# Kernel optimization log

Measured on AMD Instinct MI355X. Metric: run time of the kernel, lower is better.

The kernel has to match this reference:

```python
import jax, jax.numpy as jnp
import numpy as np
import itertools

DIM = 9  # LUT resolution per axis
B, C, H, W = 4, 5, 1024, 1024


def setup_inputs() -> dict:
    key = jax.random.key(0)
    k1, k2 = jax.random.split(key)
    x = jax.random.uniform(k1, (B, C, H, W), dtype=jnp.float32)  # pixel values in [0,1]
    LUT = jax.random.normal(k2, (1, 5, DIM, DIM, DIM, DIM, DIM), dtype=jnp.float32)
    return {"x": x, "LUT": LUT}


def _pglut_transform(x, LUT):
    # x: [B,5,H,W] in [0,1]; LUT: [1,5,dim,dim,dim,dim,dim]
    dim = LUT.shape[2]
    scale = jnp.float32(dim - 1)
    xs = x * scale                                   # [B,5,H,W]
    idx = jnp.clip(jnp.floor(xs), 0, dim - 2).astype(jnp.int32)
    frac = xs - idx.astype(x.dtype)                  # [B,5,H,W], in [0,1]

    lut_flat = LUT[0].reshape(5, dim ** 5)           # [5, dim^5]
    # flattened base index of the lower corner of the hypercube: [B,H,W]
    base = sum(idx[:, d] * int(dim ** (4 - d)) for d in range(5))

    out = jnp.zeros((5,) + base.shape, x.dtype)      # [5,B,H,W]
    for corner in itertools.product((0, 1), repeat=5):
        offset = sum(c * int(dim ** (4 - d)) for d, c in enumerate(corner))
        # quinlinear weight: prod_d (frac_d if corner else 1-frac_d)
        w = jnp.ones(base.shape, x.dtype)
        for d, c in enumerate(corner):
            w = w * (frac[:, d] if c else (1.0 - frac[:, d]))
        vals = lut_flat[:, base + offset]            # gather -> [5,B,H,W]
        out = out + w[None] * vals
    return jnp.transpose(out, (1, 0, 2, 3))          # [B,5,H,W]


def reference(x, LUT):
    return _pglut_transform(x, LUT)
```

## Files before the change

### kernel.cpp

```cpp
#include <hip/hip_runtime.h>
#include <hip/hip_fp16.h>


#define HW_    (1024 * 1024)
#define NPIX   (4 * HW_)
#define LUTC   59049
#define NBIN   512
#define CAP    8704
#define OVFCAP 65536
#define PXB    4096
#define NCELL2 (9 * 9 * 8 * 8 * 8)
#define OVF_IDX 1023

#define R_BYTES   ((size_t)NCELL2 * 80)
#define PAY_ENT   ((size_t)NBIN * CAP + OVFCAP)
#define PAY_BYTES (PAY_ENT * 16)
#define POS_BYTES ((size_t)NPIX * 4)
#define OFF_R    ((size_t)0)
#define OFF_PAY  (OFF_R + R_BYTES)
#define OFF_POS  (OFF_PAY + PAY_BYTES)
#define OFF_CNT  (OFF_POS + POS_BYTES)
#define CNT_BYTES ((size_t)4096)
#define WS_NEED  (OFF_CNT + CNT_BYTES)

typedef _Float16 v2h __attribute__((ext_vector_type(2)));
typedef float    f4v __attribute__((ext_vector_type(4)));
union H2U { __half2 h; uint u; v2h v; };
union H8U { uint4 q; __half2 h2[4]; };
union HQ8 { __half h[8]; uint4 q; };

__global__ __launch_bounds__(256) void k1_buildR(
    const float* __restrict__ lut, __half* __restrict__ R)
{
    __shared__ float s[5 * 162];
    int bid = blockIdx.x;
    int i2 = bid & 7;
    int r  = bid >> 3;
    int Q  = r * 9 + i2;
    const int fb = Q * 81;
    for (int u = threadIdx.x; u < 5 * 162; u += 256) {
        int c = u / 162; int j = u - c * 162;
        s[u] = lut[(size_t)c * LUTC + fb + j];
    }
    __syncthreads();
    int cellBaseG = bid * 64;
    for (int t = threadIdx.x; t < 320; t += 256) {
        int cell = t / 5; int c = t - cell * 5;
        int i3 = cell >> 3, i4 = cell & 7;
        const float* L = s + c * 162 + i3 * 9 + i4;
        HQ8 u;
        u.h[0] = __float2half(L[0]);   u.h[1] = __float2half(L[81]);
        u.h[2] = __float2half(L[1]);   u.h[3] = __float2half(L[82]);
        u.h[4] = __float2half(L[9]);   u.h[5] = __float2half(L[90]);
        u.h[6] = __float2half(L[10]);  u.h[7] = __float2half(L[91]);
        ((uint4*)R)[(size_t)(cellBaseG + cell) * 5 + c] = u.q;
    }
}

__global__ __launch_bounds__(1024) void k4_fused(
    const float* __restrict__ x,
    uint* __restrict__ gcnt,
    uint4* __restrict__ pay, uint* __restrict__ sortpos)
{
    __shared__ uint4  sPay[PXB];
    __shared__ uint   sStart[NBIN];
    __shared__ uint   sCur[NBIN];
    __shared__ uint   sCB[NBIN];
    __shared__ uint   sWsum[8];

    int tid = threadIdx.x, blk = blockIdx.x;
    if (tid < NBIN) sCur[tid] = 0;
    __syncthreads();

    int pBase = blk * PXB + tid * 4;
    int b = pBase >> 20, hw = pBase & (HW_ - 1);
    const float* xp = x + (size_t)b * 5 * HW_ + hw;
    f4v xv[5];
    #pragma unroll
    for (int d = 0; d < 5; ++d)
        xv[d] = __builtin_nontemporal_load((const f4v*)(xp + (size_t)d * HW_));

    uint4 plr[4]; uint keyr[4];
    #pragma unroll
    for (int j = 0; j < 4; ++j) {
        float f[5]; int idx[5];
        #pragma unroll
        for (int d = 0; d < 5; ++d) {
            float xs = xv[d][j] * 8.0f;
            int i = (int)floorf(xs); i = i < 0 ? 0 : (i > 7 ? 7 : i);
            idx[d] = i; f[d] = xs - (float)i;
        }
        int key   = (idx[0] << 6) | (idx[1] << 3) | idx[2];
        int local = (idx[3] << 3) | idx[4];
        H2U a, bq, c;
        a.h  = __float22half2_rn(make_float2(f[0], f[1]));
        bq.h = __float22half2_rn(make_float2(f[2], f[3]));
        c.h  = __float22half2_rn(make_float2(f[4], 0.f));
        plr[j].x = a.u; plr[j].y = bq.u; plr[j].z = c.u;
        plr[j].w = (uint)(pBase + j) | ((uint)local << 22);
        keyr[j] = (uint)key;
        atomicAdd(&sCur[key], 1u);
    }
    __syncthreads();

    uint v = 0, s = 0, base = 0;
    if (tid < NBIN) {
        v = sCur[tid];
        if (v) base = atomicAdd(&gcnt[tid * 2], v);
        s = v;
        #pragma unroll
        for (int off = 1; off < 64; off <<= 1) {
            uint t = __shfl_up(s, off);
            if ((tid & 63) >= off) s += t;
        }
        if ((tid & 63) == 63) sWsum[tid >> 6] = s;
    }
    __syncthreads();
    if (tid < NBIN) {
        uint add = 0;
        #pragma unroll
        for (int w = 0; w < 8; ++w)
            add += (w < (tid >> 6)) ? sWsum[w] : 0u;
        sStart[tid] = s + add - v;
        sCB[tid]    = base;
        sCur[tid]   = 0;
    }
    __syncthreads();

    uint dstr[4];
    #pragma unroll
    for (int j = 0; j < 4; ++j) {
        uint key  = keyr[j];
        uint rank = atomicAdd(&sCur[key], 1u);
        uint slot = sStart[key] + rank;
        sPay[slot] = plr[j];
        uint gIdx = sCB[key] + rank;
        uint dst;
        if (gIdx < CAP) {
            dst = key * CAP + gIdx;
        } else {
            uint oi = atomicAdd(&gcnt[OVF_IDX], 1u);
            if (oi >= OVFCAP) oi = OVFCAP - 1;
            pay[(size_t)NBIN * CAP + oi] = plr[j];
            dst = (uint)(NBIN * CAP) + oi;
        }
        dstr[j] = dst;
    }
    *(uint4*)(sortpos + pBase) = make_uint4(dstr[0], dstr[1], dstr[2], dstr[3]);
    __syncthreads();

    if (tid < NBIN) {
        uint cnt = sCur[tid];
        uint st  = sStart[tid];
        uint cb  = sCB[tid];
        uint4* gp = pay + (size_t)tid * CAP;
        #pragma unroll 2
        for (uint j = 0; j < cnt; ++j) {
            uint gIdx = cb + j;
            if (gIdx < CAP)
                gp[gIdx] = sPay[st + j];
        }
    }
}

__global__ __launch_bounds__(256, 7) void k5_compute(
    const __half* __restrict__ R, const uint* __restrict__ gcnt,
    uint4* __restrict__ pay)
{
    __shared__ uint4 stbl[1280];
    int bid = blockIdx.x;
    int bin = bid >> 2, q = bid & 3;
    int i0 = bin >> 6, i1 = (bin >> 3) & 7, i2 = bin & 7;
    const uint4* R4 = (const uint4*)R;
    #pragma unroll
    for (int slab = 0; slab < 4; ++slab) {
        int a = slab >> 1, bcorner = slab & 1;
        size_t srcBase = (size_t)((((i0 + a) * 9 + (i1 + bcorner)) * 8 + i2) * 64) * 5;
        for (int rr = threadIdx.x; rr < 320; rr += 256)
            stbl[slab * 320 + rr] = R4[srcBase + rr];
    }
    __syncthreads();
    uint n = gcnt[bin * 2]; if (n > CAP) n = CAP;
    uint B0 = (uint)bin * CAP;
    uint st = B0 + ((n * q) >> 2), en = B0 + ((n * (q + 1)) >> 2);
    for (uint i = st + threadIdx.x; i < en; i += 256) {
        uint4 pl = pay[i];
        H2U f01, f23, f4x; f01.u = pl.x; f23.u = pl.y; f4x.u = pl.z;
        float2 F01 = __half22float2(f01.h);
        float2 F23 = __half22float2(f23.h);
        float f0 = F01.x, f1 = F01.y, f2 = F23.x;
        __half2 f33 = __half2half2(__high2half(f23.h));
        __half2 f44 = __half2half2(__low2half(f4x.h));
        int local = (int)(pl.w >> 22);
        const uint4* cbase = stbl + local * 5;
        float g0 = 1.f - f0, g1 = 1.f - f1, g2 = 1.f - f2;
        H2U wv[4];
        float w00 = g0 * g1, w01c = g0 * f1, w10 = f0 * g1, w11 = f0 * f1;
        wv[0].h = __float22half2_rn(make_float2(w00  * g2, w00  * f2));
        wv[1].h = __float22half2_rn(make_float2(w01c * g2, w01c * f2));
        wv[2].h = __float22half2_rn(make_float2(w10  * g2, w10  * f2));
        wv[3].h = __float22half2_rn(make_float2(w11  * g2, w11  * f2));
        float acc[5];
        #pragma unroll
        for (int c = 0; c < 5; ++c) acc[c] = 0.f;
        #pragma unroll
        for (int slab = 0; slab < 4; ++slab) {
            #pragma unroll
            for (int c = 0; c < 5; ++c) {
                H8U u; u.q = cbase[slab * 320 + c];
                __half2 e0 = __hfma2(f44, __hsub2(u.h2[1], u.h2[0]), u.h2[0]);
                __half2 e1 = __hfma2(f44, __hsub2(u.h2[3], u.h2[2]), u.h2[2]);
                H2U dd; dd.h = __hfma2(f33, __hsub2(e1, e0), e0);
#if __has_builtin(__builtin_amdgcn_fdot2)
                acc[c] = __builtin_amdgcn_fdot2(dd.v, wv[slab].v, acc[c], false);
#else
                float2 D = __half22float2(dd.h);
                float2 W = __half22float2(wv[slab].h);
                acc[c] = fmaf(D.x, W.x, fmaf(D.y, W.y, acc[c]));
#endif
            }
        }
        H2U o01, o23, o4x;
        o01.h = __float22half2_rn(make_float2(acc[0], acc[1]));
        o23.h = __float22half2_rn(make_float2(acc[2], acc[3]));
        o4x.h = __float22half2_rn(make_float2(acc[4], 0.f));
        uint4 res; res.x = o01.u; res.y = o23.u; res.z = o4x.u; res.w = pl.w;
        pay[i] = res;
    }
}

__global__ __launch_bounds__(256) void k5_ovf(
    const float* __restrict__ x, const __half* __restrict__ R,
    const uint* __restrict__ gcnt, uint4* __restrict__ pay)
{
    uint n = gcnt[OVF_IDX]; if (n > OVFCAP) n = OVFCAP;
    for (uint i = blockIdx.x * 256 + threadIdx.x; i < n; i += 64 * 256) {
        uint4 pl = pay[(size_t)NBIN * CAP + i];
        uint p = pl.w & 0x3FFFFFu;
        int b = p >> 20, hw = p & (HW_ - 1);
        const float* xp = x + (size_t)b * 5 * HW_ + hw;
        float f[5]; int idx[5];
        #pragma unroll
        for (int d = 0; d < 5; ++d) {
            float xs = xp[(size_t)d * HW_] * 8.0f;
            int ii = (int)floorf(xs); ii = ii < 0 ? 0 : (ii > 7 ? 7 : ii);
            idx[d] = ii; f[d] = xs - (float)ii;
        }
        float g0 = 1.f - f[0], g1 = 1.f - f[1];
        float f2 = f[2], f3 = f[3], f4 = f[4];
        int cellBase = ((idx[0] * 9 + idx[1]) * 8 + idx[2]) * 64 + idx[3] * 8 + idx[4];
        float acc[5];
        #pragma unroll
        for (int c = 0; c < 5; ++c) acc[c] = 0.f;
        #pragma unroll
        for (int c0 = 0; c0 < 2; ++c0) {
            float w0 = c0 ? f[0] : g0;
            int o0 = cellBase + c0 * 4608;
            #pragma unroll
            for (int c1 = 0; c1 < 2; ++c1) {
                float w = w0 * (c1 ? f[1] : g1);
                const uint4* pc = (const uint4*)R + (size_t)(o0 + c1 * 512) * 5;
                #pragma unroll
                for (int c = 0; c < 5; ++c) {
                    HQ8 u; u.q = pc[c];
                    float e00 = __half2float(u.h[0]) + f2 * (__half2float(u.h[1]) - __half2float(u.h[0]));
                    float e01 = __half2float(u.h[2]) + f2 * (__half2float(u.h[3]) - __half2float(u.h[2]));
                    float e10 = __half2float(u.h[4]) + f2 * (__half2float(u.h[5]) - __half2float(u.h[4]));
                    float e11 = __half2float(u.h[6]) + f2 * (__half2float(u.h[7]) - __half2float(u.h[6]));
                    float d0 = e00 + f4 * (e01 - e00);
                    float d1 = e10 + f4 * (e11 - e10);
                    float vv = d0 + f3 * (d1 - d0);
                    acc[c] = fmaf(w, vv, acc[c]);
                }
            }
        }
        H2U o01, o23, o4x;
        o01.h = __float22half2_rn(make_float2(acc[0], acc[1]));
        o23.h = __float22half2_rn(make_float2(acc[2], acc[3]));
        o4x.h = __float22half2_rn(make_float2(acc[4], 0.f));
        uint4 res; res.x = o01.u; res.y = o23.u; res.z = o4x.u; res.w = pl.w;
        pay[(size_t)NBIN * CAP + i] = res;
    }
}

__global__ __launch_bounds__(1024) void k6_unpermute(
    const uint* __restrict__ sortpos, const uint4* __restrict__ res,
    float* __restrict__ out)
{
    int pBase = blockIdx.x * 4096 + threadIdx.x * 4;
    uint4 d4 = *(const uint4*)(sortpos + pBase);
    uint4 r0 = res[d4.x];
    uint4 r1 = res[d4.y];
    uint4 r2 = res[d4.z];
    uint4 r3 = res[d4.w];
    H2U a0, a1, a2, a3, b0, b1, b2, b3, c0, c1, c2, c3;
    a0.u = r0.x; b0.u = r0.y; c0.u = r0.z;
    a1.u = r1.x; b1.u = r1.y; c1.u = r1.z;
    a2.u = r2.x; b2.u = r2.y; c2.u = r2.z;
    a3.u = r3.x; b3.u = r3.y; c3.u = r3.z;
    float2 A0 = __half22float2(a0.h), A1 = __half22float2(a1.h);
    float2 A2 = __half22float2(a2.h), A3 = __half22float2(a3.h);
    float2 B0 = __half22float2(b0.h), B1 = __half22float2(b1.h);
    float2 B2 = __half22float2(b2.h), B3 = __half22float2(b3.h);
    float2 C0 = __half22float2(c0.h), C1 = __half22float2(c1.h);
    float2 C2 = __half22float2(c2.h), C3 = __half22float2(c3.h);
    int b = pBase >> 20, hw = pBase & (HW_ - 1);
    float* op = out + (size_t)b * 5 * HW_ + hw;
    f4v o;
    o[0] = A0.x; o[1] = A1.x; o[2] = A2.x; o[3] = A3.x;
    __builtin_nontemporal_store(o, (f4v*)(op));
    o[0] = A0.y; o[1] = A1.y; o[2] = A2.y; o[3] = A3.y;
    __builtin_nontemporal_store(o, (f4v*)(op + HW_));
    o[0] = B0.x; o[1] = B1.x; o[2] = B2.x; o[3] = B3.x;
    __builtin_nontemporal_store(o, (f4v*)(op + 2 * HW_));
    o[0] = B0.y; o[1] = B1.y; o[2] = B2.y; o[3] = B3.y;
    __builtin_nontemporal_store(o, (f4v*)(op + 3 * HW_));
    o[0] = C0.x; o[1] = C1.x; o[2] = C2.x; o[3] = C3.x;
    __builtin_nontemporal_store(o, (f4v*)(op + 4 * HW_));
}

__global__ __launch_bounds__(256) void buildR3(
    const float* __restrict__ lut, __half* __restrict__ R)
{
    int t = blockIdx.x * blockDim.x + threadIdx.x;
    if (t >= 5 * NCELL2) return;
    int cell = t / 5;
    int c    = t - cell * 5;
    int i4 = cell & 7;
    int i3 = (cell >> 3) & 7;
    int i2 = (cell >> 6) & 7;
    int r  = cell >> 9;
    int i1 = r % 9;
    int i0 = r / 9;
    int flat = (((i0 * 9 + i1) * 9 + i2) * 9 + i3) * 9 + i4;
    const float* qq = lut + c * LUTC + flat;
    HQ8 u;
    u.h[0] = __float2half(qq[0]);  u.h[1] = __float2half(qq[1]);
    u.h[2] = __float2half(qq[9]);  u.h[3] = __float2half(qq[10]);
    u.h[4] = __float2half(qq[81]); u.h[5] = __float2half(qq[82]);
    u.h[6] = __float2half(qq[90]); u.h[7] = __float2half(qq[91]);
    ((uint4*)R)[t] = u.q;
}

__device__ __forceinline__ float lerpf(float a, float b, float t) {
    return fmaf(t, b - a, a);
}

__global__ __launch_bounds__(256) void gather3(
    const float* __restrict__ x, const __half* __restrict__ R,
    float* __restrict__ out)
{
    int p = blockIdx.x * blockDim.x + threadIdx.x;
    if (p >= NPIX) return;
    int b  = p >> 20;
    int hw = p & (HW_ - 1);
    const float* xp = x + (size_t)b * 5 * HW_ + hw;
    float f[5], g[5]; int idx[5];
    #pragma unroll
    for (int d = 0; d < 5; ++d) {
        float xs = __builtin_nontemporal_load(xp + (size_t)d * HW_) * 8.0f;
        int i = (int)floorf(xs); i = i < 0 ? 0 : (i > 7 ? 7 : i);
        idx[d] = i; f[d] = xs - (float)i; g[d] = 1.0f - f[d];
    }
    const float f2 = f[2], f3 = f[3], f4 = f[4];
    int base = ((idx[0] * 9 + idx[1]) * 8 + idx[2]) * 64 + idx[3] * 8 + idx[4];
    float acc0 = 0.f, acc1 = 0.f, acc2 = 0.f, acc3 = 0.f, acc4 = 0.f;
    #pragma unroll
    for (int c0 = 0; c0 < 2; ++c0) {
        const float w0 = c0 ? f[0] : g[0];
        const int  o0  = base + c0 * 4608;
        #pragma unroll
        for (int c1 = 0; c1 < 2; ++c1) {
            const float w  = w0 * (c1 ? f[1] : g[1]);
            const __half* pc = R + (size_t)(o0 + c1 * 512) * 40;
            #pragma unroll
            for (int c = 0; c < 5; ++c) {
                HQ8 u; u.q = *(const uint4*)(pc + c * 8);
                float v000 = __half2float(u.h[0]);
                float v001 = __half2float(u.h[1]);
                float v010 = __half2float(u.h[2]);
                float v011 = __half2float(u.h[3]);
                float v100 = __half2float(u.h[4]);
                float v101 = __half2float(u.h[5]);
                float v110 = __half2float(u.h[6]);
                float v111 = __half2float(u.h[7]);
                float e00 = lerpf(v000, v001, f2);
                float e01 = lerpf(v010, v011, f2);
                float e10 = lerpf(v100, v101, f2);
                float e11 = lerpf(v110, v111, f2);
                float d0  = lerpf(e00, e01, f4);
                float d1  = lerpf(e10, e11, f4);
                float s   = lerpf(d0, d1, f3);
                if      (c == 0) acc0 = fmaf(w, s, acc0);
                else if (c == 1) acc1 = fmaf(w, s, acc1);
                else if (c == 2) acc2 = fmaf(w, s, acc2);
                else if (c == 3) acc3 = fmaf(w, s, acc3);
                else             acc4 = fmaf(w, s, acc4);
            }
        }
    }
    float* op = out + (size_t)b * 5 * HW_ + hw;
    __builtin_nontemporal_store(acc0, op + 0 * HW_);
    __builtin_nontemporal_store(acc1, op + 1 * HW_);
    __builtin_nontemporal_store(acc2, op + 2 * HW_);
    __builtin_nontemporal_store(acc3, op + 3 * HW_);
    __builtin_nontemporal_store(acc4, op + 4 * HW_);
}

extern "C" void kernel_launch(void* const* d_in, const int* in_sizes, int n_in,
                              void* d_out, int out_size, void* d_ws, size_t ws_size,
                              hipStream_t stream)
{
    const float* x   = (const float*)d_in[0];
    const float* lut = (const float*)d_in[1];
    float* out       = (float*)d_out;
    char* ws         = (char*)d_ws;

    if (ws != nullptr && ws_size >= WS_NEED) {
        __half* R      = (__half*)(ws + OFF_R);
        uint4*  pay    = (uint4*)(ws + OFF_PAY);
        uint*   sortp  = (uint*)(ws + OFF_POS);
        uint*   gcnt   = (uint*)(ws + OFF_CNT);

        hipMemsetAsync(gcnt, 0, CNT_BYTES, stream);
        k1_buildR   <<<648, 256, 0, stream>>>(lut, R);
        k4_fused    <<<NPIX / PXB, 1024, 0, stream>>>(x, gcnt, pay, sortp);
        k5_compute  <<<4 * NBIN, 256, 0, stream>>>(R, gcnt, pay);
        k5_ovf      <<<64, 256, 0, stream>>>(x, R, gcnt, pay);
        k6_unpermute<<<NPIX / 4096, 1024, 0, stream>>>(sortp, pay, out);
    } else if (ws != nullptr && ws_size >= R_BYTES) {
        __half* R = (__half*)ws;
        int nb = (5 * NCELL2 + 255) / 256;
        buildR3<<<nb, 256, 0, stream>>>(lut, R);
        gather3<<<NPIX / 256, 256, 0, stream>>>(x, R, out);
    }
}
```

Before: 246.6 us.

## Process two tiles per block in binning kernel with prefetch and split scatter

The binning kernel now handles two 4096-pixel tiles per block, issuing the second tile's input loads while the first tile is being binned. This hides global load latency behind the shared-memory histogram work. The final scatter of staged payloads to global bins is split across all 1024 threads (two halves per bin) instead of only 512. Launch bounds gain a min-blocks hint, and the grid is halved. In exchange the kernel holds more registers per thread and runs fewer blocks with extra barriers.

```diff
diff --git a/kernel.cpp b/kernel.cpp
--- a/kernel.cpp
+++ b/kernel.cpp
@@ -57,7 +57,7 @@
     }
 }
 
-__global__ __launch_bounds__(1024) void k4_fused(
+__global__ __launch_bounds__(1024, 8) void k4_fused(
     const float* __restrict__ x,
     uint* __restrict__ gcnt,
     uint4* __restrict__ pay, uint* __restrict__ sortpos)
@@ -68,97 +68,119 @@
     __shared__ uint   sCB[NBIN];
     __shared__ uint   sWsum[8];
 
-    int tid = threadIdx.x, blk = blockIdx.x;
-    if (tid < NBIN) sCur[tid] = 0;
-    __syncthreads();
-
-    int pBase = blk * PXB + tid * 4;
-    int b = pBase >> 20, hw = pBase & (HW_ - 1);
-    const float* xp = x + (size_t)b * 5 * HW_ + hw;
-    f4v xv[5];
+    int tid = threadIdx.x;
+    int tile0 = blockIdx.x * 2;
+
+    f4v xv[2][5];
+    {
+        int pB = tile0 * PXB + tid * 4;
+        int b = pB >> 20, hw = pB & (HW_ - 1);
+        const float* xp = x + (size_t)b * 5 * HW_ + hw;
+        #pragma unroll
+        for (int d = 0; d < 5; ++d)
+            xv[0][d] = __builtin_nontemporal_load((const f4v*)(xp + (size_t)d * HW_));
+    }
+
     #pragma unroll
-    for (int d = 0; d < 5; ++d)
-        xv[d] = __builtin_nontemporal_load((const f4v*)(xp + (size_t)d * HW_));
-
-    uint4 plr[4]; uint keyr[4];
-    #pragma unroll
-    for (int j = 0; j < 4; ++j) {
-        float f[5]; int idx[5];
-        #pragma unroll
-        for (int d = 0; d < 5; ++d) {
-            float xs = xv[d][j] * 8.0f;
-            int i = (int)floorf(xs); i = i < 0 ? 0 : (i > 7 ? 7 : i);
-            idx[d] = i; f[d] = xs - (float)i;
-        }
-        int key   = (idx[0] << 6) | (idx[1] << 3) | idx[2];
-        int local = (idx[3] << 3) | idx[4];
-        H2U a, bq, c;
-        a.h  = __float22half2_rn(make_float2(f[0], f[1]));
-        bq.h = __float22half2_rn(make_float2(f[2], f[3]));
-        c.h  = __float22half2_rn(make_float2(f[4], 0.f));
-        plr[j].x = a.u; plr[j].y = bq.u; plr[j].z = c.u;
-        plr[j].w = (uint)(pBase + j) | ((uint)local << 22);
-        keyr[j] = (uint)key;
-        atomicAdd(&sCur[key], 1u);
-    }
-    __syncthreads();
-
-    uint v = 0, s = 0, base = 0;
-    if (tid < NBIN) {
-        v = sCur[tid];
-        if (v) base = atomicAdd(&gcnt[tid * 2], v);
-        s = v;
-        #pragma unroll
-        for (int off = 1; off < 64; off <<= 1) {
-            uint t = __shfl_up(s, off);
-            if ((tid & 63) >= off) s += t;
-        }
-        if ((tid & 63) == 63) sWsum[tid >> 6] = s;
-    }
-    __syncthreads();
-    if (tid < NBIN) {
-        uint add = 0;
-        #pragma unroll
-        for (int w = 0; w < 8; ++w)
-            add += (w < (tid >> 6)) ? sWsum[w] : 0u;
-        sStart[tid] = s + add - v;
-        sCB[tid]    = base;
-        sCur[tid]   = 0;
-    }
-    __syncthreads();
-
-    uint dstr[4];
-    #pragma unroll
-    for (int j = 0; j < 4; ++j) {
-        uint key  = keyr[j];
-        uint rank = atomicAdd(&sCur[key], 1u);
-        uint slot = sStart[key] + rank;
-        sPay[slot] = plr[j];
-        uint gIdx = sCB[key] + rank;
-        uint dst;
-        if (gIdx < CAP) {
-            dst = key * CAP + gIdx;
-        } else {
-            uint oi = atomicAdd(&gcnt[OVF_IDX], 1u);
-            if (oi >= OVFCAP) oi = OVFCAP - 1;
-            pay[(size_t)NBIN * CAP + oi] = plr[j];
-            dst = (uint)(NBIN * CAP) + oi;
-        }
-        dstr[j] = dst;
-    }
-    *(uint4*)(sortpos + pBase) = make_uint4(dstr[0], dstr[1], dstr[2], dstr[3]);
-    __syncthreads();
-
-    if (tid < NBIN) {
-        uint cnt = sCur[tid];
-        uint st  = sStart[tid];
-        uint cb  = sCB[tid];
-        uint4* gp = pay + (size_t)tid * CAP;
-        #pragma unroll 2
-        for (uint j = 0; j < cnt; ++j) {
-            uint gIdx = cb + j;
-            if (gIdx < CAP)
-                gp[gIdx] = sPay[st + j];
+    for (int t = 0; t < 2; ++t) {
+        int pBase = (tile0 + t) * PXB + tid * 4;
+
+        __syncthreads();
+        if (tid < NBIN) sCur[tid] = 0;
+        __syncthreads();
+
+        uint4 plr[4]; uint keyr[4];
+        #pragma unroll
+        for (int j = 0; j < 4; ++j) {
+            float f[5]; int idx[5];
+            #pragma unroll
+            for (int d = 0; d < 5; ++d) {
+                float xs = xv[t][d][j] * 8.0f;
+                int i = (int)floorf(xs); i = i < 0 ? 0 : (i > 7 ? 7 : i);
+                idx[d] = i; f[d] = xs - (float)i;
+            }
+            int key   = (idx[0] << 6) | (idx[1] << 3) | idx[2];
+            int local = (idx[3] << 3) | idx[4];
+            H2U a, bq, c;
+            a.h  = __float22half2_rn(make_float2(f[0], f[1]));
+            bq.h = __float22half2_rn(make_float2(f[2], f[3]));
+            c.h  = __float22half2_rn(make_float2(f[4], 0.f));
+            plr[j].x = a.u; plr[j].y = bq.u; plr[j].z = c.u;
+            plr[j].w = (uint)(pBase + j) | ((uint)local << 22);
+            keyr[j] = (uint)key;
+            atomicAdd(&sCur[keyr[j]], 1u);
+        }
+
+        if (t == 0) {
+            int pB = (tile0 + 1) * PXB + tid * 4;
+            int b = pB >> 20, hw = pB & (HW_ - 1);
+            const float* xp = x + (size_t)b * 5 * HW_ + hw;
+            #pragma unroll
+            for (int d = 0; d < 5; ++d)
+                xv[1][d] = __builtin_nontemporal_load((const f4v*)(xp + (size_t)d * HW_));
+        }
+        __syncthreads();
+
+        uint v = 0, s = 0, base = 0;
+        if (tid < NBIN) {
+            v = sCur[tid];
+            if (v) base = atomicAdd(&gcnt[tid * 2], v);
+            s = v;
+            #pragma unroll
+            for (int off = 1; off < 64; off <<= 1) {
+                uint tt = __shfl_up(s, off);
+                if ((tid & 63) >= off) s += tt;
+            }
+            if ((tid & 63) == 63) sWsum[tid >> 6] = s;
+        }
+        __syncthreads();
+        if (tid < NBIN) {
+            uint add = 0;
+            #pragma unroll
+            for (int w = 0; w < 8; ++w)
+                add += (w < (tid >> 6)) ? sWsum[w] : 0u;
+            sStart[tid] = s + add - v;
+            sCB[tid]    = base;
+            sCur[tid]   = 0;
+        }
+        __syncthreads();
+
+        uint dstr[4];
+        #pragma unroll
+        for (int j = 0; j < 4; ++j) {
+            uint key  = keyr[j];
+            uint rank = atomicAdd(&sCur[key], 1u);
+            uint slot = sStart[key] + rank;
+            sPay[slot] = plr[j];
+            uint gIdx = sCB[key] + rank;
+            uint dst;
+            if (gIdx < CAP) {
+                dst = key * CAP + gIdx;
+            } else {
+                uint oi = atomicAdd(&gcnt[OVF_IDX], 1u);
+                if (oi >= OVFCAP) oi = OVFCAP - 1;
+                pay[(size_t)NBIN * CAP + oi] = plr[j];
+                dst = (uint)(NBIN * CAP) + oi;
+            }
+            dstr[j] = dst;
+        }
+        *(uint4*)(sortpos + pBase) = make_uint4(dstr[0], dstr[1], dstr[2], dstr[3]);
+        __syncthreads();
+
+        {
+            uint bin  = tid & (NBIN - 1);
+            uint half = tid >> 9;
+            uint cnt = sCur[bin];
+            uint st  = sStart[bin];
+            uint cb  = sCB[bin];
+            uint j0  = (cnt * half) >> 1;
+            uint j1  = (cnt * (half + 1)) >> 1;
+            uint4* gp = pay + (size_t)bin * CAP;
+            for (uint j = j0; j < j1; ++j) {
+                uint gIdx = cb + j;
+                if (gIdx < CAP)
+                    gp[gIdx] = sPay[st + j];
+            }
         }
     }
 }
@@ -424,7 +446,7 @@
 
         hipMemsetAsync(gcnt, 0, CNT_BYTES, stream);
         k1_buildR   <<<648, 256, 0, stream>>>(lut, R);
-        k4_fused    <<<NPIX / PXB, 1024, 0, stream>>>(x, gcnt, pay, sortp);
+        k4_fused    <<<NPIX / PXB / 2, 1024, 0, stream>>>(x, gcnt, pay, sortp);
         k5_compute  <<<4 * NBIN, 256, 0, stream>>>(R, gcnt, pay);
         k5_ovf      <<<64, 256, 0, stream>>>(x, R, gcnt, pay);
         k6_unpermute<<<NPIX / 4096, 1024, 0, stream>>>(sortp, pay, out);
```

After: 265.6 us. 1.08x slower.
